# Performance work log

Hardware: AMD Instinct MI355X
Metric: run time of the kernel (lower is better)

Reference implementation:

```python
import jax, jax.numpy as jnp
import numpy as np

TEMPERATURE = 0.1
BASE_TEMPERATURE = 1.0
LAMBDA_CTR = 1.0
NUM_CLASS = 12
N_VIEWS = 2
EPS_NORM = 1e-12   # F.normalize eps
EPS_POS = 1e-6     # denominator eps on mask.sum


def _graph():
    # binarized tridiagonal AU adjacency (adjacent_matrix after > pcc_threshold -> 1)
    i = jnp.arange(NUM_CLASS)
    return (jnp.abs(i[:, None] - i[None, :]) <= 1).astype(jnp.float32)


def setup_inputs() -> dict:
    key = jax.random.key(0)
    k1, k2 = jax.random.split(key)
    B, d = 512, 4096
    features = jax.random.normal(k1, (B, N_VIEWS, NUM_CLASS, d), dtype=jnp.float32)
    outputs = jax.random.normal(k2, (B, NUM_CLASS), dtype=jnp.float32)
    targets = jax.random.randint(jax.random.fold_in(key, 7), (B, NUM_CLASS), 0, 2, dtype=jnp.int32)
    return {"outputs": outputs, "targets": targets, "features": features}


def reference(outputs, targets, features):
    B = features.shape[0]
    M = N_VIEWS * NUM_CLASS  # anchors per sample
    # per-sample feature rows, L2 normalized (F.normalize, dim=1)
    f = features.reshape(B, M, -1)
    f = f / jnp.clip(jnp.linalg.norm(f, axis=-1, keepdims=True), EPS_NORM)
    # cosine-similarity logits / temperature: [B, M, M]
    logits = jnp.einsum('bmd,bnd->bmn', f, f) / TEMPERATURE
    logits_mask = 1.0 - jnp.eye(M, dtype=jnp.float32)      # drop self-contrast
    mask = jnp.tile(_graph(), (N_VIEWS, N_VIEWS)) * logits_mask  # positives
    # masked log-softmax denominator (is_stable=False: no max subtraction)
    exp_logits = jnp.exp(logits) * logits_mask
    log_prob = logits - jnp.log(exp_logits.sum(-1, keepdims=True))
    mean_log_prob_pos = (mask * log_prob).sum(-1) / (mask.sum(-1) + EPS_POS)  # [B, M]
    per_sample = (-(TEMPERATURE / BASE_TEMPERATURE) * mean_log_prob_pos).mean(-1)  # [B]
    return LAMBDA_CTR * per_sample.sum() / B
```

## Files before the change

kernel.cpp:

```cpp
#include <hip/hip_runtime.h>
#include <math.h>


#define MROWS 24
#define DIM   4096
#define CH    256
#define NCH   (DIM / CH)
#define NPAIR 300
#define PPW   75

typedef float f32x4 __attribute__((ext_vector_type(4)));

constexpr int pair_i(int p) {
    int i = 0;
    while (p >= MROWS - i) { p -= MROWS - i; ++i; }
    return i;
}
constexpr int pair_j(int p) {
    int i = 0;
    while (p >= MROWS - i) { p -= MROWS - i; ++i; }
    return i + p;
}

__device__ __forceinline__ void gll16(const float* g, float* l) {
    __builtin_amdgcn_global_load_lds(
        (const __attribute__((address_space(1))) unsigned int*)g,
        (__attribute__((address_space(3))) unsigned int*)l, 16, 0, 0);
}

template<int W, int P>
__device__ __forceinline__ void accum_pairs(const f32x4* f, float* acc) {
    if constexpr (P < PPW) {
        constexpr int gp = W * PPW + P;
        constexpr int i = pair_i(gp);
        constexpr int j = pair_j(gp);
        #pragma unroll
        for (int s = 0; s < 4; ++s)
            acc[P] = fmaf(f[i][s], f[j][s], acc[P]);
        accum_pairs<W, P + 1>(f, acc);
    }
}

template<int W>
__device__ __forceinline__ void accum_chunk(const float* tile, int lane, float* acc) {
    f32x4 f[MROWS];
    #pragma unroll
    for (int r = 0; r < MROWS; ++r)
        f[r] = *(const f32x4*)(tile + r * CH + lane * 4);
    accum_pairs<W, 0>(f, acc);
}

__global__ __launch_bounds__(256, 2)
void brc_loss_kernel(const float* __restrict__ F, float* __restrict__ out, float scale) {
    __shared__ float tile[2][MROWS * CH];
    __shared__ float Gf[MROWS * MROWS];
    __shared__ float inv_n[MROWS];
    __shared__ float rowv[MROWS];

    const int tid  = threadIdx.x;
    const int lane = tid & 63;
    const int wave = tid >> 6;
    const int b    = blockIdx.x;
    const float* base = F + (size_t)b * (MROWS * DIM);

    float acc[PPW];
    #pragma unroll
    for (int p = 0; p < PPW; ++p) acc[p] = 0.0f;

    {
        const float* src = base + lane * 4;
        #pragma unroll
        for (int q = 0; q < 6; ++q) {
            const int r = wave * 6 + q;
            gll16(src + (size_t)r * DIM, &tile[0][r * CH]);
        }
    }
    __syncthreads();

    int cur = 0;
    for (int k = 0; k < NCH; ++k) {
        if (k + 1 < NCH) {
            const float* src = base + (k + 1) * CH + lane * 4;
            #pragma unroll
            for (int q = 0; q < 6; ++q) {
                const int r = wave * 6 + q;
                gll16(src + (size_t)r * DIM, &tile[cur ^ 1][r * CH]);
            }
        }
        switch (wave) {
            case 0:  accum_chunk<0>(tile[cur], lane, acc); break;
            case 1:  accum_chunk<1>(tile[cur], lane, acc); break;
            case 2:  accum_chunk<2>(tile[cur], lane, acc); break;
            default: accum_chunk<3>(tile[cur], lane, acc); break;
        }
        __syncthreads();
        cur ^= 1;
    }

    #pragma unroll
    for (int p = 0; p < PPW; ++p) {
        float v = acc[p];
        #pragma unroll
        for (int off = 32; off; off >>= 1)
            v += __shfl_xor(v, off, 64);
        if (lane == 0) {
            int gp = wave * PPW + p;
            int i = 0, rem = gp;
            while (rem >= MROWS - i) { rem -= MROWS - i; ++i; }
            int j = i + rem;
            Gf[i * MROWS + j] = v;
            Gf[j * MROWS + i] = v;
        }
    }
    __syncthreads();

    if (tid < MROWS)
        inv_n[tid] = 1.0f / fmaxf(sqrtf(Gf[tid * MROWS + tid]), 1e-12f);
    __syncthreads();

    if (tid < MROWS) {
        const int i = tid;
        const int ci = i % 12;
        const float inv_i = inv_n[i];
        float denom = 0.0f, possum = 0.0f;
        int cnt = 0;
        for (int j = 0; j < MROWS; ++j) {
            if (j == i) continue;
            float l = Gf[i * MROWS + j] * inv_i * inv_n[j] * (1.0f / 0.1f);
            denom += expf(l);
            int cj = j % 12;
            int dc = ci - cj; if (dc < 0) dc = -dc;
            if (dc <= 1) { possum += l; ++cnt; }
        }
        float mean = (possum - (float)cnt * logf(denom)) / ((float)cnt + 1e-6f);
        rowv[i] = -0.1f * mean;
    }
    __syncthreads();

    if (tid == 0) {
        float s = 0.0f;
        #pragma unroll
        for (int i = 0; i < MROWS; ++i) s += rowv[i];
        atomicAdd(out, s * scale);
    }
}

extern "C" void kernel_launch(void* const* d_in, const int* in_sizes, int n_in,
                              void* d_out, int out_size, void* d_ws, size_t ws_size,
                              hipStream_t stream) {
    (void)n_in; (void)d_ws; (void)ws_size; (void)out_size;
    const float* F = (const float*)d_in[2];
    float* out = (float*)d_out;
    const int B = in_sizes[2] / (2 * 12 * DIM);
    const float scale = 1.0f / (24.0f * (float)B);

    hipMemsetAsync(d_out, 0, sizeof(float), stream);
    brc_loss_kernel<<<dim3(B), dim3(256), 0, stream>>>(F, out, scale);
}
```

Measured before the change: 334.9 us.

## Deepen LDS prefetch to triple buffering with explicit vmcnt waits

```diff
diff --git a/kernel.cpp b/kernel.cpp
--- a/kernel.cpp
+++ b/kernel.cpp
@@ -6,7 +6,7 @@
 #define DIM   4096
 #define CH    256
 #define NCH   (DIM / CH)
-#define NPAIR 300
+#define DEPTH 3
 #define PPW   75
 
 typedef float f32x4 __attribute__((ext_vector_type(4)));
@@ -27,6 +27,11 @@
         (const __attribute__((address_space(1))) unsigned int*)g,
         (__attribute__((address_space(3))) unsigned int*)l, 16, 0, 0);
 }
+
+#define WAITV(N) do { \
+    asm volatile("s_waitcnt vmcnt(" #N ")" ::: "memory"); \
+    __builtin_amdgcn_sched_barrier(0); \
+} while (0)
 
 template<int W, int P>
 __device__ __forceinline__ void accum_pairs(const f32x4* f, float* acc) {
@@ -52,7 +57,7 @@
 
 __global__ __launch_bounds__(256, 2)
 void brc_loss_kernel(const float* __restrict__ F, float* __restrict__ out, float scale) {
-    __shared__ float tile[2][MROWS * CH];
+    __shared__ float tile[DEPTH][MROWS * CH];
     __shared__ float Gf[MROWS * MROWS];
     __shared__ float inv_n[MROWS];
     __shared__ float rowv[MROWS];
@@ -60,41 +65,42 @@
     const int tid  = threadIdx.x;
     const int lane = tid & 63;
     const int wave = tid >> 6;
-    const int b    = blockIdx.x;
-    const float* base = F + (size_t)b * (MROWS * DIM);
+    const float* base = F + (size_t)blockIdx.x * (MROWS * DIM);
 
     float acc[PPW];
     #pragma unroll
     for (int p = 0; p < PPW; ++p) acc[p] = 0.0f;
 
-    {
-        const float* src = base + lane * 4;
+    auto issue = [&](int k) {
+        const float* src = base + k * CH + lane * 4;
+        float* dst = &tile[k % DEPTH][0];
         #pragma unroll
         for (int q = 0; q < 6; ++q) {
             const int r = wave * 6 + q;
-            gll16(src + (size_t)r * DIM, &tile[0][r * CH]);
+            gll16(src + (size_t)r * DIM, dst + r * CH);
         }
-    }
-    __syncthreads();
+    };
 
-    int cur = 0;
+    issue(0); issue(1); issue(2);
+
+    #pragma unroll 1
     for (int k = 0; k < NCH; ++k) {
-        if (k + 1 < NCH) {
-            const float* src = base + (k + 1) * CH + lane * 4;
-            #pragma unroll
-            for (int q = 0; q < 6; ++q) {
-                const int r = wave * 6 + q;
-                gll16(src + (size_t)r * DIM, &tile[cur ^ 1][r * CH]);
-            }
+        if (k < NCH - 2)       WAITV(12);
+        else if (k == NCH - 2) WAITV(6);
+        else                   WAITV(0);
+        __builtin_amdgcn_s_barrier();
+        __builtin_amdgcn_sched_barrier(0);
+
+        const float* t = &tile[k % DEPTH][0];
+        switch (wave) {
+            case 0:  accum_chunk<0>(t, lane, acc); break;
+            case 1:  accum_chunk<1>(t, lane, acc); break;
+            case 2:  accum_chunk<2>(t, lane, acc); break;
+            default: accum_chunk<3>(t, lane, acc); break;
         }
-        switch (wave) {
-            case 0:  accum_chunk<0>(tile[cur], lane, acc); break;
-            case 1:  accum_chunk<1>(tile[cur], lane, acc); break;
-            case 2:  accum_chunk<2>(tile[cur], lane, acc); break;
-            default: accum_chunk<3>(tile[cur], lane, acc); break;
-        }
-        __syncthreads();
-        cur ^= 1;
+        __builtin_amdgcn_sched_barrier(0);
+        __builtin_amdgcn_s_barrier();
+        if (k + DEPTH < NCH) issue(k + DEPTH);
     }
 
     #pragma unroll
```

New measurement: 335.0 us. Within noise of the previous version (+0.0%).
